# Optimization experiments

Measured on AMD Instinct MI355X. Metric: run time of the kernel, lower is better.

Reference implementation:

```python
import jax, jax.numpy as jnp
import numpy as np

T, B, I, H = 512, 64, 1024, 1024
STD = 1.0 / np.sqrt(H)  # reset_parameters: uniform(-std, std) on all params


def setup_inputs() -> dict:
    key = jax.random.key(0)
    ks = jax.random.split(key, 6)
    u = lambda k, shape: jax.random.uniform(k, shape, jnp.float32, -STD, STD)
    return {
        "input_": jax.random.normal(ks[0], (T, B, I), jnp.float32),
        "h0": jnp.zeros((B, H), jnp.float32),
        "c0": jnp.zeros((B, H), jnp.float32),
        "weight_ih": u(ks[1], (4 * H, I)),
        "weight_hh": u(ks[2], (4 * H, H)),
        "bias_ih": u(ks[3], (4 * H,)),
        "bias_hh": u(ks[4], (4 * H,)),
        "retention_ratio": u(ks[5], (H,)),
    }


def reference(input_, h0, c0, weight_ih, weight_hh, bias_ih, bias_hh, retention_ratio):
    # Precompute input-side gate projections for all timesteps: [T, B, 4H]
    x_gates = jnp.einsum('tbi,gi->tbg', input_, weight_ih) + bias_ih + bias_hh
    r = retention_ratio

    def step(carry, xg):
        h, c = carry
        gates = xg + h @ weight_hh.T  # [B, 4H]
        i, f, g, o = jnp.split(gates, 4, axis=1)
        cy = jax.nn.sigmoid(f) * c + jax.nn.sigmoid(i) * jnp.tanh(g)
        hy = jax.nn.sigmoid(o) * jnp.tanh(cy)
        hy = r * h + (1.0 - r) * hy  # low-pass blend
        return (hy, cy), hy

    (hT, cT), outputs = jax.lax.scan(step, (h0, c0), x_gates)
    return outputs, hT, cT
```

## Files before the change

### kernel.cpp

```cpp
#include <hip/hip_runtime.h>
#include <hip/hip_bf16.h>
#include <math.h>

#define T_STEPS 512
#define BATCH   64
#define IN_DIM  1024
#define HID     1024
#define G4      (4 * HID)
#define MTOT    (T_STEPS * BATCH)
#define TBH     ((size_t)T_STEPS * BATCH * HID)

#define BM 128
#define BN 128
#define BK 16
#define LDT 132

__global__ __launch_bounds__(256) void xgemm_kernel(
    const float* __restrict__ A, const float* __restrict__ W,
    const float* __restrict__ bih, const float* __restrict__ bhh,
    float* __restrict__ C) {
  __shared__ float As[BK][LDT];
  __shared__ float Ws[BK][LDT];
  const int tid = threadIdx.x;
  const int m0 = blockIdx.y * BM;
  const int n0 = blockIdx.x * BN;
  const int tx = tid & 15, ty = tid >> 4;
  const int srow = tid >> 2;
  const int scol = (tid & 3) << 2;

  float acc[8][8];
#pragma unroll
  for (int i = 0; i < 8; ++i)
#pragma unroll
    for (int j = 0; j < 8; ++j) acc[i][j] = 0.f;

  const float* Ap0 = A + (size_t)(m0 + srow) * IN_DIM + scol;
  const float* Ap1 = Ap0 + (size_t)64 * IN_DIM;
  const float* Wp0 = W + (size_t)(n0 + srow) * IN_DIM + scol;
  const float* Wp1 = Wp0 + (size_t)64 * IN_DIM;

  for (int k0 = 0; k0 < IN_DIM; k0 += BK) {
    float4 av0 = *(const float4*)(Ap0 + k0);
    float4 av1 = *(const float4*)(Ap1 + k0);
    float4 wv0 = *(const float4*)(Wp0 + k0);
    float4 wv1 = *(const float4*)(Wp1 + k0);
    As[scol + 0][srow]      = av0.x; As[scol + 1][srow]      = av0.y;
    As[scol + 2][srow]      = av0.z; As[scol + 3][srow]      = av0.w;
    As[scol + 0][srow + 64] = av1.x; As[scol + 1][srow + 64] = av1.y;
    As[scol + 2][srow + 64] = av1.z; As[scol + 3][srow + 64] = av1.w;
    Ws[scol + 0][srow]      = wv0.x; Ws[scol + 1][srow]      = wv0.y;
    Ws[scol + 2][srow]      = wv0.z; Ws[scol + 3][srow]      = wv0.w;
    Ws[scol + 0][srow + 64] = wv1.x; Ws[scol + 1][srow + 64] = wv1.y;
    Ws[scol + 2][srow + 64] = wv1.z; Ws[scol + 3][srow + 64] = wv1.w;
    __syncthreads();
#pragma unroll
    for (int k = 0; k < BK; ++k) {
      float4 a0 = *(const float4*)&As[k][ty * 8];
      float4 a1 = *(const float4*)&As[k][ty * 8 + 4];
      float4 w0 = *(const float4*)&Ws[k][tx * 8];
      float4 w1 = *(const float4*)&Ws[k][tx * 8 + 4];
      float a8[8] = {a0.x, a0.y, a0.z, a0.w, a1.x, a1.y, a1.z, a1.w};
      float w8[8] = {w0.x, w0.y, w0.z, w0.w, w1.x, w1.y, w1.z, w1.w};
#pragma unroll
      for (int i = 0; i < 8; ++i)
#pragma unroll
        for (int j = 0; j < 8; ++j)
          acc[i][j] = fmaf(a8[i], w8[j], acc[i][j]);
    }
    __syncthreads();
  }

  float bj[8];
#pragma unroll
  for (int j = 0; j < 8; ++j)
    bj[j] = bih[n0 + tx * 8 + j] + bhh[n0 + tx * 8 + j];
#pragma unroll
  for (int i = 0; i < 8; ++i) {
    float* cp = C + (size_t)(m0 + ty * 8 + i) * G4 + n0 + tx * 8;
    float4 s0 = make_float4(acc[i][0] + bj[0], acc[i][1] + bj[1],
                            acc[i][2] + bj[2], acc[i][3] + bj[3]);
    float4 s1 = make_float4(acc[i][4] + bj[4], acc[i][5] + bj[5],
                            acc[i][6] + bj[6], acc[i][7] + bj[7]);
    *(float4*)cp = s0;
    *(float4*)(cp + 4) = s1;
  }
}

#define NBLK 256
#define BAR_STRIDE 320

__device__ __forceinline__ float sigm(float x) {
  return 1.f / (1.f + __expf(-x));
}
__device__ __forceinline__ float tanh_(float x) {
  return 2.f / (1.f + __expf(-2.f * x)) - 1.f;
}

__device__ __forceinline__ void gridbar(unsigned int* base) {
  __syncthreads();
  if (threadIdx.x == 0) {
    __threadfence();
    unsigned int* leaf = base + (blockIdx.x & 15) * 16;
    unsigned int lv = __hip_atomic_fetch_add(leaf, 1u, __ATOMIC_RELAXED,
                                             __HIP_MEMORY_SCOPE_AGENT);
    if (lv == (NBLK / 16) - 1) {
      unsigned int rv = __hip_atomic_fetch_add(base + 256, 1u, __ATOMIC_RELAXED,
                                               __HIP_MEMORY_SCOPE_AGENT);
      if (rv == 15u)
        __hip_atomic_store(base + 257, 1u, __ATOMIC_RELAXED,
                           __HIP_MEMORY_SCOPE_AGENT);
    }
    while (!__hip_atomic_load(base + 257, __ATOMIC_RELAXED,
                              __HIP_MEMORY_SCOPE_AGENT)) {
      __builtin_amdgcn_s_sleep(2);
    }
    __threadfence();
  }
  __syncthreads();
}

__global__ __launch_bounds__(512) void recur_kernel(
    const float* __restrict__ xg,
    const float* __restrict__ Whh,
    const float* __restrict__ h0, const float* __restrict__ c0,
    const float* __restrict__ ret,
    float* __restrict__ out,
    unsigned int* __restrict__ bar) {
  extern __shared__ float smem[];
  float* Wlds = smem;
  float* part = smem + 32768;

  const int tid = threadIdx.x;
  const int cg = blockIdx.x >> 1;
  const int bh = blockIdx.x & 1;
  const int colbase = cg * 8;
  const int b0 = bh * 32;
  const int lane = tid & 63;
  const int wv = tid >> 6;
  const int rg = lane & 7;
  const int kc = lane >> 3;

  {
    const int row_loc = tid >> 4;
    const int kq = tid & 15;
    const int g = row_loc >> 3, colz = row_loc & 7;
    const float* wrow =
        Whh + (size_t)(g * HID + colbase + colz) * HID + kq * 64;
    const int rowbyte = ((row_loc >> 2) << 4) + ((row_loc & 3) << 2);
#pragma unroll 4
    for (int k4 = 0; k4 < 64; k4 += 4) {
      float4 w4 = *(const float4*)(wrow + k4);
      float vals[4] = {w4.x, w4.y, w4.z, w4.w};
#pragma unroll
      for (int q = 0; q < 4; ++q) {
        int k = kq * 64 + k4 + q;
        int s = (k ^ (k >> 7)) & 7;
        *(float*)((char*)Wlds + (((k << 7) + rowbyte) ^ (s << 4))) = vals[q];
      }
    }
  }

  const int ucol = tid & 7;
  const int ubl = tid >> 3;
  float c_reg = 0.f, h_reg = 0.f, r_coef = 0.f;
  if (tid < 256) {
    int gb = b0 + ubl, gc = colbase + ucol;
    c_reg = c0[gb * HID + gc];
    h_reg = h0[gb * HID + gc];
    r_coef = ret[gc];
  }
  const int uw = ubl >> 2, ubb = ubl & 3;

  __syncthreads();

  for (int t = 0; t < T_STEPS; ++t) {
    const float* hsrc =
        (t == 0) ? h0 : (out + (size_t)(t - 1) * BATCH * HID);
    const int kct = (kc + t) & 7;
    const int kcbase = kct * 128;
    const int kctx = kct << 4;
    const float* hb = hsrc + (size_t)(b0 + (wv << 2)) * HID + kcbase;

    float xgv[4];
    if (tid < 256) {
      const float* xp =
          xg + ((size_t)t * BATCH + b0 + ubl) * G4 + colbase + ucol;
#pragma unroll
      for (int q = 0; q < 4; ++q) xgv[q] = xp[q * HID];
    }

    float acc[4][4];
#pragma unroll
    for (int r = 0; r < 4; ++r)
#pragma unroll
      for (int b = 0; b < 4; ++b) acc[r][b] = 0.f;

    for (int kk = 0; kk < 128; kk += 4) {
      float ha[4][4];
      *(float4*)&ha[0][0] = *(const float4*)(hb + 0 * HID + kk);
      *(float4*)&ha[1][0] = *(const float4*)(hb + 1 * HID + kk);
      *(float4*)&ha[2][0] = *(const float4*)(hb + 2 * HID + kk);
      *(float4*)&ha[3][0] = *(const float4*)(hb + 3 * HID + kk);
#pragma unroll
      for (int q = 0; q < 4; ++q) {
        int k = kcbase + kk + q;
        int addr = (k << 7) + ((rg << 4) ^ ((((kk + q) & 7) << 4) ^ kctx));
        float wa[4];
        *(float4*)wa = *(const float4*)((const char*)Wlds + addr);
#pragma unroll
        for (int r = 0; r < 4; ++r)
#pragma unroll
          for (int b = 0; b < 4; ++b)
            acc[r][b] = fmaf(wa[r], ha[b][q], acc[r][b]);
      }
    }

#pragma unroll
    for (int r = 0; r < 4; ++r)
#pragma unroll
      for (int b = 0; b < 4; ++b) {
        float v = acc[r][b];
        v += __shfl_xor(v, 8, 64);
        v += __shfl_xor(v, 16, 64);
        v += __shfl_xor(v, 32, 64);
        acc[r][b] = v;
      }
    if (lane < 8) {
#pragma unroll
      for (int r = 0; r < 4; ++r) {
        int row = lane * 4 + r;
#pragma unroll
        for (int b = 0; b < 4; ++b) part[(wv * 32 + row) * 5 + b] = acc[r][b];
      }
    }
    __syncthreads();

    if (tid < 256) {
      float g[4];
#pragma unroll
      for (int q = 0; q < 4; ++q)
        g[q] = part[(uw * 32 + q * 8 + ucol) * 5 + ubb] + xgv[q];
      float ig = sigm(g[0]);
      float fg = sigm(g[1]);
      float gg = tanh_(g[2]);
      float og = sigm(g[3]);
      float cy = fg * c_reg + ig * gg;
      float hy = og * tanh_(cy);
      hy = r_coef * h_reg + (1.f - r_coef) * hy;
      c_reg = cy;
      h_reg = hy;
      size_t oidx = ((size_t)t * BATCH + b0 + ubl) * HID + colbase + ucol;
      out[oidx] = hy;
      if (t == T_STEPS - 1) {
        size_t tb = TBH + (size_t)(b0 + ubl) * HID + colbase + ucol;
        out[tb] = hy;
        out[tb + (size_t)BATCH * HID] = cy;
      }
    }

    if (t + 1 < T_STEPS) {
      gridbar(bar + (size_t)t * BAR_STRIDE);
    }
  }
}

extern "C" void kernel_launch(void* const* d_in, const int* in_sizes, int n_in,
                              void* d_out, int out_size, void* d_ws,
                              size_t ws_size, hipStream_t stream) {
  const float* input = (const float*)d_in[0];
  const float* h0    = (const float*)d_in[1];
  const float* c0    = (const float*)d_in[2];
  const float* wih   = (const float*)d_in[3];
  const float* whh   = (const float*)d_in[4];
  const float* bih   = (const float*)d_in[5];
  const float* bhh   = (const float*)d_in[6];
  const float* ret   = (const float*)d_in[7];
  float* out = (float*)d_out;

  unsigned int* bar = (unsigned int*)d_ws;
  float* xg = (float*)((char*)d_ws + (1 << 20));

  hipMemsetAsync(d_ws, 0, (size_t)T_STEPS * BAR_STRIDE * 4, stream);

  dim3 g1(G4 / BN, MTOT / BM);
  xgemm_kernel<<<g1, 256, 0, stream>>>(input, wih, bih, bhh, xg);

  const size_t recur_lds = (32768 + 8 * 32 * 5) * sizeof(float);
  recur_kernel<<<NBLK, 512, recur_lds, stream>>>(xg, whh, h0, c0, ret, out,
                                                 bar);
}
```

Measured before the change: 15.78 ms.

## Retile recurrent matvec: split K across two wave halves, 8 batches per wave

Restructures the per-step h·Whh^T product in the persistent recurrent kernel. Each wave now covers 8 batch rows (instead of 4) over half of K, so every LDS weight load feeds twice as many FMAs, and weight reads use a simple lane-linear addressing with a new LDS layout. Partial sums from the two K halves are combined in the gate-update phase through a padded shared buffer. This cuts LDS traffic per FMA and simplifies address math, at the cost of more accumulator registers and more global h loads per wave.

After: 18.18 ms. 1.15x slower.

```diff
diff --git a/kernel.cpp b/kernel.cpp
--- a/kernel.cpp
+++ b/kernel.cpp
@@ -137,26 +137,27 @@
   const int b0 = bh * 32;
   const int lane = tid & 63;
   const int wv = tid >> 6;
+  const int khalf = wv & 1;
+  const int oct = wv >> 1;
   const int rg = lane & 7;
   const int kc = lane >> 3;
 
   {
-    const int row_loc = tid >> 4;
-    const int kq = tid & 15;
-    const int g = row_loc >> 3, colz = row_loc & 7;
-    const float* wrow =
-        Whh + (size_t)(g * HID + colbase + colz) * HID + kq * 64;
-    const int rowbyte = ((row_loc >> 2) << 4) + ((row_loc & 3) << 2);
-#pragma unroll 4
+    const int row_loc = tid & 31;
+    const int kq = tid >> 5;
+    const int gate = row_loc >> 3, colz = row_loc & 7;
+    const int rgw = row_loc >> 2, rr = row_loc & 3;
+    const float* wrow = Whh + (size_t)(gate * HID + colbase + colz) * HID;
     for (int k4 = 0; k4 < 64; k4 += 4) {
-      float4 w4 = *(const float4*)(wrow + k4);
-      float vals[4] = {w4.x, w4.y, w4.z, w4.w};
-#pragma unroll
-      for (int q = 0; q < 4; ++q) {
-        int k = kq * 64 + k4 + q;
-        int s = (k ^ (k >> 7)) & 7;
-        *(float*)((char*)Wlds + (((k << 7) + rowbyte) ^ (s << 4))) = vals[q];
-      }
+      const int k = kq * 64 + k4;
+      float4 w = *(const float4*)(wrow + k);
+      float vals[4] = {w.x, w.y, w.z, w.w};
+      const int q = k >> 2;
+      const int base = (k >> 9) * 65536 + ((((q >> 3) & 15) * 4) << 10) +
+                       ((q & 7) << 7) + (rgw << 4) + (rr << 2);
+#pragma unroll
+      for (int e = 0; e < 4; ++e)
+        *(float*)((char*)Wlds + base + (e << 10)) = vals[e];
     }
   }
 
@@ -169,17 +170,16 @@
     h_reg = h0[gb * HID + gc];
     r_coef = ret[gc];
   }
-  const int uw = ubl >> 2, ubb = ubl & 3;
+
+  const char* wbase = (const char*)Wlds + khalf * 65536 + lane * 16;
+  const int qbase = khalf * 128 + kc;
 
   __syncthreads();
 
   for (int t = 0; t < T_STEPS; ++t) {
     const float* hsrc =
         (t == 0) ? h0 : (out + (size_t)(t - 1) * BATCH * HID);
-    const int kct = (kc + t) & 7;
-    const int kcbase = kct * 128;
-    const int kctx = kct << 4;
-    const float* hb = hsrc + (size_t)(b0 + (wv << 2)) * HID + kcbase;
+    const float4* hq = (const float4*)(hsrc + (size_t)(b0 + oct * 8) * HID);
 
     float xgv[4];
     if (tid < 256) {
@@ -189,36 +189,37 @@
       for (int q = 0; q < 4; ++q) xgv[q] = xp[q * HID];
     }
 
-    float acc[4][4];
+    const char* wb = wbase;
+    asm volatile("" : "+v"(wb));
+
+    float acc[4][8];
 #pragma unroll
     for (int r = 0; r < 4; ++r)
 #pragma unroll
-      for (int b = 0; b < 4; ++b) acc[r][b] = 0.f;
-
-    for (int kk = 0; kk < 128; kk += 4) {
-      float ha[4][4];
-      *(float4*)&ha[0][0] = *(const float4*)(hb + 0 * HID + kk);
-      *(float4*)&ha[1][0] = *(const float4*)(hb + 1 * HID + kk);
-      *(float4*)&ha[2][0] = *(const float4*)(hb + 2 * HID + kk);
-      *(float4*)&ha[3][0] = *(const float4*)(hb + 3 * HID + kk);
-#pragma unroll
-      for (int q = 0; q < 4; ++q) {
-        int k = kcbase + kk + q;
-        int addr = (k << 7) + ((rg << 4) ^ ((((kk + q) & 7) << 4) ^ kctx));
+      for (int b = 0; b < 8; ++b) acc[r][b] = 0.f;
+
+#pragma unroll 4
+    for (int j = 0; j < 16; ++j) {
+      float4 ha[8];
+#pragma unroll
+      for (int b = 0; b < 8; ++b)
+        ha[b] = hq[(size_t)b * 256 + qbase + 8 * j];
+#pragma unroll
+      for (int e = 0; e < 4; ++e) {
         float wa[4];
-        *(float4*)wa = *(const float4*)((const char*)Wlds + addr);
+        *(float4*)wa = *(const float4*)(wb + ((j * 4 + e) << 10));
 #pragma unroll
         for (int r = 0; r < 4; ++r)
 #pragma unroll
-          for (int b = 0; b < 4; ++b)
-            acc[r][b] = fmaf(wa[r], ha[b][q], acc[r][b]);
+          for (int b = 0; b < 8; ++b)
+            acc[r][b] = fmaf(wa[r], ((const float*)&ha[b])[e], acc[r][b]);
       }
     }
 
 #pragma unroll
     for (int r = 0; r < 4; ++r)
 #pragma unroll
-      for (int b = 0; b < 4; ++b) {
+      for (int b = 0; b < 8; ++b) {
         float v = acc[r][b];
         v += __shfl_xor(v, 8, 64);
         v += __shfl_xor(v, 16, 64);
@@ -227,19 +228,20 @@
       }
     if (lane < 8) {
 #pragma unroll
-      for (int r = 0; r < 4; ++r) {
-        int row = lane * 4 + r;
-#pragma unroll
-        for (int b = 0; b < 4; ++b) part[(wv * 32 + row) * 5 + b] = acc[r][b];
-      }
+      for (int r = 0; r < 4; ++r)
+#pragma unroll
+        for (int b = 0; b < 8; ++b)
+          part[(khalf * 32 + lane * 4 + r) * 33 + oct * 8 + b] = acc[r][b];
     }
     __syncthreads();
 
     if (tid < 256) {
       float g[4];
 #pragma unroll
-      for (int q = 0; q < 4; ++q)
-        g[q] = part[(uw * 32 + q * 8 + ucol) * 5 + ubb] + xgv[q];
+      for (int q = 0; q < 4; ++q) {
+        int row = q * 8 + ucol;
+        g[q] = part[row * 33 + ubl] + part[(32 + row) * 33 + ubl] + xgv[q];
+      }
       float ig = sigm(g[0]);
       float fg = sigm(g[1]);
       float gg = tanh_(g[2]);
@@ -285,7 +287,7 @@
   dim3 g1(G4 / BN, MTOT / BM);
   xgemm_kernel<<<g1, 256, 0, stream>>>(input, wih, bih, bhh, xg);
 
-  const size_t recur_lds = (32768 + 8 * 32 * 5) * sizeof(float);
+  const size_t recur_lds = (32768 + 2 * 32 * 33) * sizeof(float);
   recur_kernel<<<NBLK, 512, recur_lds, stream>>>(xg, whh, h0, c0, ret, out,
                                                  bar);
 }
```
